# Kernel tuning notes

Hardware: AMD Instinct MI355X
Metric: run time of the kernel (lower is better)

Reference implementation:

```python
import jax, jax.numpy as jnp
import numpy as np
import math

B, S, D = 2, 2048, 1024
H, HKV, HD = 16, 4, 64
SF = 4
SD = HD // SF  # sparsity proj dim = 16
TEMP = 1.0
INIT_STD = 0.02


def rope(qk):
    # qk: [b, h, s, d]
    d = qk.shape[-1]
    theta = 1.0 / (10000.0 ** (jnp.arange(0, d, 2, dtype=jnp.float32) / d))  # [d/2]
    s = jnp.arange(qk.shape[2], dtype=jnp.float32)
    freqs = jnp.outer(s, theta)                     # [s, d/2]
    freqs = jnp.concatenate([freqs, freqs], -1)     # [s, d]
    qk1, qk2 = jnp.split(qk, 2, axis=-1)
    rot = jnp.concatenate([-qk2, qk1], -1)
    return qk * jnp.cos(freqs) + rot * jnp.sin(freqs)


def setup_inputs() -> dict:
    key = jax.random.key(0)
    ks = jax.random.split(key, 8)
    x = jax.random.normal(ks[0], (B, S, D), dtype=jnp.float32)
    Wq = jax.random.normal(ks[1], (D, D), dtype=jnp.float32) * INIT_STD
    Wk = jax.random.normal(ks[2], (HKV * HD, D), dtype=jnp.float32) * INIT_STD
    Wv = jax.random.normal(ks[3], (HKV * HD, D), dtype=jnp.float32) * INIT_STD
    Wo = jax.random.normal(ks[4], (D, D), dtype=jnp.float32) * INIT_STD
    bo = jnp.zeros((D,), dtype=jnp.float32)
    Ws = jax.random.normal(ks[5], (SD, HD), dtype=jnp.float32) * INIT_STD
    bs = jnp.zeros((SD,), dtype=jnp.float32)
    return {"x": x, "Wq": Wq, "Wk": Wk, "Wv": Wv, "Wo": Wo, "bo": bo, "Ws": Ws, "bs": bs}


def reference(x, Wq, Wk, Wv, Wo, bo, Ws, bs):
    b, s, _ = x.shape
    # projections (torch Linear: x @ W.T)
    q = (x @ Wq.T).reshape(b, s, H, HD).transpose(0, 2, 1, 3)     # [b,H,s,hd]
    k = (x @ Wk.T).reshape(b, s, HKV, HD).transpose(0, 2, 1, 3)   # [b,Hkv,s,hd]
    v = (x @ Wv.T).reshape(b, s, HKV, HD).transpose(0, 2, 1, 3)
    q = rope(q)
    k = rope(k)
    n_rep = H // HKV
    k = jnp.repeat(k, n_rep, axis=1)  # [b,H,s,hd]
    v = jnp.repeat(v, n_rep, axis=1)
    # low-rank sparsity gate
    q_sp = q @ Ws.T + bs              # [b,H,s,sd]
    k_sp = k @ Ws.T + bs
    sp_scores = jnp.einsum('bhid,bhjd->bhij', q_sp, k_sp) / math.sqrt(SD)
    gate = jax.nn.sigmoid(sp_scores / TEMP)
    attn = jnp.einsum('bhid,bhjd->bhij', q, k) / math.sqrt(HD)
    attn = attn * gate
    causal = jnp.triu(jnp.ones((s, s), dtype=bool), k=1)
    attn = jnp.where(causal, -jnp.inf, attn)
    w = jax.nn.softmax(attn, axis=-1)
    out = jnp.einsum('bhij,bhjd->bhid', w, v)               # [b,H,s,hd]
    out = out.transpose(0, 2, 1, 3).reshape(b, s, H * HD)   # [b,s,D]
    return out @ Wo.T + bo
```

## Files before the change

### kernel.cpp

```cpp
#include <hip/hip_runtime.h>
#include <math.h>

#define B_ 2
#define S_ 2048
#define D_ 1024
#define H_ 16
#define HKV_ 4
#define HD_ 64
#define SD_ 16

typedef __attribute__((ext_vector_type(8))) short bf16x8;
typedef __attribute__((ext_vector_type(4))) float f32x4;
typedef __attribute__((ext_vector_type(8))) unsigned short us8;
typedef __attribute__((ext_vector_type(4))) unsigned short us4;

__device__ __forceinline__ unsigned short f2bf(float f) {
  unsigned int u = __builtin_bit_cast(unsigned int, f);
  u += 0x7fffu + ((u >> 16) & 1u);
  return (unsigned short)(u >> 16);
}

__device__ __forceinline__ void gload16(const unsigned short* g, unsigned short* l) {
  __builtin_amdgcn_global_load_lds(
      (const __attribute__((address_space(1))) unsigned int*)g,
      (__attribute__((address_space(3))) unsigned int*)l, 16, 0, 0);
}

__global__ __launch_bounds__(256) void convert_bf16(
    const float* __restrict__ x, const float* __restrict__ wq,
    const float* __restrict__ wk, const float* __restrict__ wv,
    const float* __restrict__ wo, unsigned short* __restrict__ xb,
    unsigned short* __restrict__ wqkv, unsigned short* __restrict__ wob) {
  const int blk = blockIdx.x;
  const float* src;
  unsigned short* dst;
  int off;
  if (blk < 2048)      { src = x;  dst = xb;             off = blk * 2048; }
  else if (blk < 2560) { src = wq; dst = wqkv;           off = (blk - 2048) * 2048; }
  else if (blk < 2688) { src = wk; dst = wqkv + 1048576; off = (blk - 2560) * 2048; }
  else if (blk < 2816) { src = wv; dst = wqkv + 1310720; off = (blk - 2688) * 2048; }
  else                 { src = wo; dst = wob;            off = (blk - 2816) * 2048; }
  const int i = off + threadIdx.x * 8;
  float4 a = *(const float4*)(src + i);
  float4 b = *(const float4*)(src + i + 4);
  us8 o;
  o[0] = f2bf(a.x); o[1] = f2bf(a.y); o[2] = f2bf(a.z); o[3] = f2bf(a.w);
  o[4] = f2bf(b.x); o[5] = f2bf(b.y); o[6] = f2bf(b.z); o[7] = f2bf(b.w);
  *(us8*)(dst + i) = o;
}

__global__ __launch_bounds__(256) void gemm_bf16(
    const unsigned short* __restrict__ A, const unsigned short* __restrict__ Bm,
    const float* __restrict__ bias, float* __restrict__ C, int N) {
  __shared__ unsigned short As[128 * 64];
  __shared__ unsigned short Bs[128 * 64];
  const int tid = threadIdx.x;
  const int w = tid >> 6, lane = tid & 63;
  const int nm = lane & 15, quad = lane >> 4;
  const int m0 = blockIdx.y * 128, n0 = blockIdx.x * 128;
  const int wm = (w & 1) * 64, wn = (w >> 1) * 64;

  f32x4 acc[4][4] = {};
  int srow[4], scol[4];
#pragma unroll
  for (int it = 0; it < 4; ++it) {
    int s = it * 256 + w * 64 + lane;
    srow[it] = s >> 3;
    scol[it] = ((s & 7) ^ (srow[it] & 7)) * 8;
  }

  for (int k0 = 0; k0 < 1024; k0 += 64) {
    __syncthreads();
#pragma unroll
    for (int it = 0; it < 4; ++it)
      gload16(A + (size_t)(m0 + srow[it]) * 1024 + k0 + scol[it],
              &As[(it * 256 + w * 64) * 8]);
#pragma unroll
    for (int it = 0; it < 4; ++it)
      gload16(Bm + (size_t)(n0 + srow[it]) * 1024 + k0 + scol[it],
              &Bs[(it * 256 + w * 64) * 8]);
    __syncthreads();

#pragma unroll
    for (int ks = 0; ks < 2; ++ks) {
      bf16x8 af[4], bf[4];
      const int cq = ks * 4 + quad;
#pragma unroll
      for (int mi = 0; mi < 4; ++mi) {
        const int m = wm + mi * 16 + nm;
        af[mi] = *(const bf16x8*)&As[(m * 8 + (cq ^ (m & 7))) * 8];
      }
#pragma unroll
      for (int ni = 0; ni < 4; ++ni) {
        const int n = wn + ni * 16 + nm;
        bf[ni] = *(const bf16x8*)&Bs[(n * 8 + (cq ^ (n & 7))) * 8];
      }
#pragma unroll
      for (int mi = 0; mi < 4; ++mi)
#pragma unroll
        for (int ni = 0; ni < 4; ++ni)
          acc[mi][ni] = __builtin_amdgcn_mfma_f32_16x16x32_bf16(
              af[mi], bf[ni], acc[mi][ni], 0, 0, 0);
    }
  }

  float bv[4] = {0.f, 0.f, 0.f, 0.f};
  if (bias) {
#pragma unroll
    for (int ni = 0; ni < 4; ++ni) bv[ni] = bias[n0 + wn + ni * 16 + nm];
  }
#pragma unroll
  for (int mi = 0; mi < 4; ++mi) {
#pragma unroll
    for (int r = 0; r < 4; ++r) {
      const int row = m0 + wm + mi * 16 + quad * 4 + r;
      float* crow = C + (size_t)row * N + n0 + wn + nm;
#pragma unroll
      for (int ni = 0; ni < 4; ++ni) crow[ni * 16] = acc[mi][ni][r] + bv[ni];
    }
  }
}

__global__ __launch_bounds__(256) void rope_scatter(
    const float* __restrict__ P, const float* __restrict__ Ws,
    const float* __restrict__ bs, unsigned short* __restrict__ qh,
    unsigned short* __restrict__ kh, unsigned short* __restrict__ qsp,
    unsigned short* __restrict__ ksp) {
  __shared__ float wsl[16 * 64];
  __shared__ float bsl[16];
  __shared__ float rbuf[4][64];
  const int tid = threadIdx.x;
  const int row = blockIdx.x;
  const int b = row >> 11;
  const int s = row & 2047;
  {
    *(float4*)&wsl[tid * 4] = *(const float4*)&Ws[tid * 4];
    if (tid < 16) bsl[tid] = bs[tid];
  }
  __syncthreads();
  const int w = tid >> 6, lane = tid & 63;
  const int i = lane & 31, halfu = lane >> 5;
  const float theta = powf(10000.f, -((float)(2 * i) * (1.f / 64.f)));
  const float f = (float)s * theta;
  const float cf = cosf(f);
  const float sf = sinf(f);
  for (int slot = w; slot < 20; slot += 4) {
    float val = P[(size_t)row * 1536 + slot * 64 + lane];
    float partner = __shfl_xor(val, 32);
    float rot = halfu ? partner : -partner;
    float r = val * cf + rot * sf;
    unsigned short* dst;
    unsigned short* spdst;
    float qscale, spscale;
    if (slot < 16) {
      dst = qh + ((size_t)(b * 16 + slot) * 2048 + s) * 64;
      spdst = qsp + ((size_t)(b * 16 + slot) * 2048 + s) * 16;
      qscale = 0.125f; spscale = 0.25f;
    } else {
      int hh = slot - 16;
      dst = kh + ((size_t)(b * 4 + hh) * 2048 + s) * 64;
      spdst = ksp + ((size_t)(b * 4 + hh) * 2048 + s) * 16;
      qscale = 1.f; spscale = 1.f;
    }
    dst[lane] = f2bf(r * qscale);
    rbuf[w][lane] = r;
    int p = lane >> 4, j = lane & 15;
    float partial = 0.f;
#pragma unroll
    for (int t = 0; t < 16; ++t)
      partial += wsl[j * 64 + p * 16 + t] * rbuf[w][p * 16 + t];
    partial += __shfl_xor(partial, 16);
    partial += __shfl_xor(partial, 32);
    if (p == 0) spdst[j] = f2bf((partial + bsl[j]) * spscale);
  }
}

__global__ __launch_bounds__(256) void v_transpose(
    const float* __restrict__ proj, unsigned short* __restrict__ vt) {
  __shared__ unsigned short t_[64 * 72];
  const int bkv = blockIdx.y;
  const int s0 = blockIdx.x * 64;
  const int b = bkv >> 2, hkv = bkv & 3;
  const int tid = threadIdx.x;
  const int sl = tid >> 2;
  const int c0 = (tid & 3) * 16;
  const float* src = proj + ((size_t)b * 2048 + s0 + sl) * 1536 + 1280 + hkv * 64 + c0;
  us8 o0, o1;
#pragma unroll
  for (int t = 0; t < 8; ++t) { o0[t] = f2bf(src[t]); o1[t] = f2bf(src[8 + t]); }
  *(us8*)&t_[sl * 72 + c0] = o0;
  *(us8*)&t_[sl * 72 + c0 + 8] = o1;
  __syncthreads();
  const int d = tid >> 2;
  const int sc_ = (tid & 3) * 16;
  us8 w0, w1;
#pragma unroll
  for (int t = 0; t < 8; ++t) w0[t] = t_[(sc_ + t) * 72 + d];
#pragma unroll
  for (int t = 0; t < 8; ++t) w1[t] = t_[(sc_ + 8 + t) * 72 + d];
  unsigned short* dst = vt + (size_t)bkv * 131072 + (size_t)d * 2048 + s0 + sc_;
  *(us8*)dst = w0;
  *(us8*)(dst + 8) = w1;
}

__global__ __launch_bounds__(256) void attn_kernel(
    const unsigned short* __restrict__ qh, const unsigned short* __restrict__ kh,
    const unsigned short* __restrict__ vt, const unsigned short* __restrict__ qsp,
    const unsigned short* __restrict__ ksp, unsigned short* __restrict__ ao) {
  __shared__ unsigned short Ks[64 * 64];
  __shared__ unsigned short Vs[64 * 64];
  __shared__ unsigned short Ksp[64 * 16];
  __shared__ unsigned short Pw[4][16 * 64];

  const int tid = threadIdx.x;
  const int w = tid >> 6;
  const int lane = tid & 63;
  const int nm = lane & 15;
  const int quad = lane >> 4;
  const int bh = blockIdx.y;
  const int b = bh >> 4, h = bh & 15;
  const int hkv = h >> 2;
  const size_t kbase = (size_t)(b * 4 + hkv) * 2048 * 64;
  const size_t vbase = (size_t)(b * 4 + hkv) * 131072;
  const size_t kspb = (size_t)(b * 4 + hkv) * 2048 * 16;

  int srow_[2], scol_[2];
#pragma unroll
  for (int rd = 0; rd < 2; ++rd) {
    int Lc = rd * 256 + w * 64 + lane;
    int r = Lc >> 3;
    srow_[rd] = r;
    scol_[rd] = ((Lc & 7) ^ (r & 7)) * 8;
  }
  unsigned short* pw = &Pw[w][0];

  for (int ph = 0; ph < 2; ++ph) {
    const int qx = ph ? blockIdx.x : (31 - blockIdx.x);
    const int q0 = qx * 64;
    const int qrow0 = q0 + w * 16;

    const size_t qb = ((size_t)(b * 16 + h) * 2048 + qrow0 + nm) * 64;
    bf16x8 qa0 = *(const bf16x8*)(qh + qb + quad * 8);
    bf16x8 qa1 = *(const bf16x8*)(qh + qb + 32 + quad * 8);
    bf16x8 qspa = {0, 0, 0, 0, 0, 0, 0, 0};
    if (quad < 2)
      qspa = *(const bf16x8*)(qsp + ((size_t)(b * 16 + h) * 2048 + qrow0 + nm) * 16 + quad * 8);

    float l_r[4] = {0.f, 0.f, 0.f, 0.f};
    f32x4 O[4] = {{0.f, 0.f, 0.f, 0.f}, {0.f, 0.f, 0.f, 0.f},
                  {0.f, 0.f, 0.f, 0.f}, {0.f, 0.f, 0.f, 0.f}};

    const int ntile = qx + 1;
    for (int jt = 0; jt < ntile; ++jt) {
      const int j0 = jt * 64;
      __syncthreads();
#pragma unroll
      for (int rd = 0; rd < 2; ++rd) {
        gload16(kh + kbase + (size_t)(j0 + srow_[rd]) * 64 + scol_[rd],
                &Ks[(rd * 256 + w * 64) * 8]);
        gload16(vt + vbase + (size_t)srow_[rd] * 2048 + j0 + scol_[rd],
                &Vs[(rd * 256 + w * 64) * 8]);
      }
      if (w < 2) {
        const int Lc = w * 64 + lane;
        gload16(ksp + kspb + (size_t)(j0 + (Lc >> 1)) * 16 + (Lc & 1) * 8,
                &Ksp[w * 512]);
      }
      __syncthreads();

      const bool needmask = (j0 + 63 > qrow0);
#pragma unroll
      for (int st = 0; st < 4; ++st) {
        const int krow = st * 16 + nm;
        const int r7 = krow & 7;
        bf16x8 kb0 = *(const bf16x8*)&Ks[(krow * 8 + (quad ^ r7)) * 8];
        bf16x8 kb1 = *(const bf16x8*)&Ks[(krow * 8 + ((4 + quad) ^ r7)) * 8];
        bf16x8 gb = *(const bf16x8*)&Ksp[(krow * 2 + (quad & 1)) * 8];
        f32x4 z = {0.f, 0.f, 0.f, 0.f};
        f32x4 s = __builtin_amdgcn_mfma_f32_16x16x32_bf16(qa0, kb0, z, 0, 0, 0);
        s = __builtin_amdgcn_mfma_f32_16x16x32_bf16(qa1, kb1, s, 0, 0, 0);
        f32x4 g = __builtin_amdgcn_mfma_f32_16x16x32_bf16(qspa, gb, z, 0, 0, 0);
#pragma unroll
        for (int r = 0; r < 4; ++r) {
          float gate = 1.f / (1.f + __expf(-g[r]));
          float v = s[r] * gate;
          if (needmask) {
            const int col = j0 + st * 16 + nm;
            const int rowg = qrow0 + quad * 4 + r;
            v = (col > rowg) ? -INFINITY : v;
          }
          float p = __expf(v);
          l_r[r] += p;
          const int prow = quad * 4 + r;
          const int chunk = (st * 2 + (nm >> 3)) ^ (prow & 7);
          pw[(prow * 8 + chunk) * 8 + (nm & 7)] = f2bf(p);
        }
      }

#pragma unroll
      for (int c = 0; c < 2; ++c) {
        const int gc = c * 4 + quad;
        bf16x8 pa = *(const bf16x8*)&pw[(nm * 8 + (gc ^ (nm & 7))) * 8];
#pragma unroll
        for (int dt = 0; dt < 4; ++dt) {
          const int vrow = dt * 16 + nm;
          bf16x8 vb = *(const bf16x8*)&Vs[(vrow * 8 + (gc ^ (vrow & 7))) * 8];
          O[dt] = __builtin_amdgcn_mfma_f32_16x16x32_bf16(pa, vb, O[dt], 0, 0, 0);
        }
      }
    }

#pragma unroll
    for (int r = 0; r < 4; ++r) {
      float v = l_r[r];
      v += __shfl_xor(v, 1);
      v += __shfl_xor(v, 2);
      v += __shfl_xor(v, 4);
      v += __shfl_xor(v, 8);
      const float inv = 1.f / v;
      const int rowg = qrow0 + quad * 4 + r;
      unsigned short* orow = ao + ((size_t)b * 2048 + rowg) * 1024 + h * 64 + nm;
#pragma unroll
      for (int dt = 0; dt < 4; ++dt) orow[dt * 16] = f2bf(O[dt][r] * inv);
    }
  }
}

extern "C" void kernel_launch(void* const* d_in, const int* in_sizes, int n_in,
                              void* d_out, int out_size, void* d_ws,
                              size_t ws_size, hipStream_t stream) {
  const float* x = (const float*)d_in[0];
  const float* Wq = (const float*)d_in[1];
  const float* Wk = (const float*)d_in[2];
  const float* Wv = (const float*)d_in[3];
  const float* Wo = (const float*)d_in[4];
  const float* bo = (const float*)d_in[5];
  const float* Ws = (const float*)d_in[6];
  const float* bs = (const float*)d_in[7];
  float* out = (float*)d_out;

  char* wsb = (char*)d_ws;
  float* proj = (float*)wsb;
  unsigned short* aob = (unsigned short*)wsb;
  unsigned short* qh   = (unsigned short*)(wsb + 25165824);
  unsigned short* kh   = (unsigned short*)(wsb + 33554432);
  unsigned short* vtb  = (unsigned short*)(wsb + 35651584);
  unsigned short* qsp  = (unsigned short*)(wsb + 37748736);
  unsigned short* ksp  = (unsigned short*)(wsb + 39845888);
  unsigned short* xb   = (unsigned short*)(wsb + 40370176);
  unsigned short* wqkv = (unsigned short*)(wsb + 48758784);
  unsigned short* wob  = (unsigned short*)(wsb + 51904512);

  convert_bf16<<<dim3(3328), 256, 0, stream>>>(x, Wq, Wk, Wv, Wo, xb, wqkv, wob);
  gemm_bf16<<<dim3(12, 32), 256, 0, stream>>>(xb, wqkv, nullptr, proj, 1536);
  rope_scatter<<<dim3(4096), 256, 0, stream>>>(proj, Ws, bs, qh, kh, qsp, ksp);
  v_transpose<<<dim3(32, 8), 256, 0, stream>>>(proj, vtb);
  attn_kernel<<<dim3(16, 32), 256, 0, stream>>>(qh, kh, vtb, qsp, ksp, aob);
  gemm_bf16<<<dim3(8, 32), 256, 0, stream>>>(aob, wob, bo, out, 1024);
}
```

Baseline: 226.8 us.

## Shrink GEMM tiles, split attention into one q-tile per block, use exp2

The GEMM block tile drops from 128x128 to 64x128, with each wave now covering 64x32, which doubles the grid to fill more compute units. The attention kernel no longer has each block process two paired q-tiles in sequence; it launches one block per q-tile, interleaving small and large tiles by block index to spread the causal work. The log2(e) factor is folded into the q and sparsity-q scales so the kernel can call exp2f instead of __expf. The trade-off is less operand reuse per GEMM block and possible load imbalance between attention blocks in exchange for more parallelism.

```diff
diff --git a/kernel.cpp b/kernel.cpp
--- a/kernel.cpp
+++ b/kernel.cpp
@@ -13,6 +13,8 @@
 typedef __attribute__((ext_vector_type(4))) float f32x4;
 typedef __attribute__((ext_vector_type(8))) unsigned short us8;
 typedef __attribute__((ext_vector_type(4))) unsigned short us4;
+
+#define LOG2E 1.4426950408889634f
 
 __device__ __forceinline__ unsigned short f2bf(float f) {
   unsigned int u = __builtin_bit_cast(unsigned int, f);
@@ -52,71 +54,77 @@
 __global__ __launch_bounds__(256) void gemm_bf16(
     const unsigned short* __restrict__ A, const unsigned short* __restrict__ Bm,
     const float* __restrict__ bias, float* __restrict__ C, int N) {
-  __shared__ unsigned short As[128 * 64];
+  __shared__ unsigned short As[64 * 64];
   __shared__ unsigned short Bs[128 * 64];
   const int tid = threadIdx.x;
   const int w = tid >> 6, lane = tid & 63;
   const int nm = lane & 15, quad = lane >> 4;
-  const int m0 = blockIdx.y * 128, n0 = blockIdx.x * 128;
-  const int wm = (w & 1) * 64, wn = (w >> 1) * 64;
-
-  f32x4 acc[4][4] = {};
-  int srow[4], scol[4];
+  const int m0 = blockIdx.y * 64, n0 = blockIdx.x * 128;
+  const int wn = w * 32;
+
+  f32x4 acc[4][2] = {};
+  int arow[2], acol[2], brow[4], bcol[4];
+#pragma unroll
+  for (int it = 0; it < 2; ++it) {
+    int s = it * 256 + tid;
+    arow[it] = s >> 3;
+    acol[it] = ((s & 7) ^ (arow[it] & 7)) * 8;
+  }
 #pragma unroll
   for (int it = 0; it < 4; ++it) {
-    int s = it * 256 + w * 64 + lane;
-    srow[it] = s >> 3;
-    scol[it] = ((s & 7) ^ (srow[it] & 7)) * 8;
+    int s = it * 256 + tid;
+    brow[it] = s >> 3;
+    bcol[it] = ((s & 7) ^ (brow[it] & 7)) * 8;
   }
 
   for (int k0 = 0; k0 < 1024; k0 += 64) {
     __syncthreads();
 #pragma unroll
+    for (int it = 0; it < 2; ++it)
+      gload16(A + (size_t)(m0 + arow[it]) * 1024 + k0 + acol[it],
+              &As[(it * 256 + w * 64) * 8]);
+#pragma unroll
     for (int it = 0; it < 4; ++it)
-      gload16(A + (size_t)(m0 + srow[it]) * 1024 + k0 + scol[it],
-              &As[(it * 256 + w * 64) * 8]);
-#pragma unroll
-    for (int it = 0; it < 4; ++it)
-      gload16(Bm + (size_t)(n0 + srow[it]) * 1024 + k0 + scol[it],
+      gload16(Bm + (size_t)(n0 + brow[it]) * 1024 + k0 + bcol[it],
               &Bs[(it * 256 + w * 64) * 8]);
     __syncthreads();
 
 #pragma unroll
     for (int ks = 0; ks < 2; ++ks) {
-      bf16x8 af[4], bf[4];
       const int cq = ks * 4 + quad;
+      bf16x8 af[4], bfr[2];
 #pragma unroll
       for (int mi = 0; mi < 4; ++mi) {
-        const int m = wm + mi * 16 + nm;
+        const int m = mi * 16 + nm;
         af[mi] = *(const bf16x8*)&As[(m * 8 + (cq ^ (m & 7))) * 8];
       }
 #pragma unroll
-      for (int ni = 0; ni < 4; ++ni) {
+      for (int ni = 0; ni < 2; ++ni) {
         const int n = wn + ni * 16 + nm;
-        bf[ni] = *(const bf16x8*)&Bs[(n * 8 + (cq ^ (n & 7))) * 8];
+        bfr[ni] = *(const bf16x8*)&Bs[(n * 8 + (cq ^ (n & 7))) * 8];
       }
 #pragma unroll
       for (int mi = 0; mi < 4; ++mi)
 #pragma unroll
-        for (int ni = 0; ni < 4; ++ni)
+        for (int ni = 0; ni < 2; ++ni)
           acc[mi][ni] = __builtin_amdgcn_mfma_f32_16x16x32_bf16(
-              af[mi], bf[ni], acc[mi][ni], 0, 0, 0);
-    }
-  }
-
-  float bv[4] = {0.f, 0.f, 0.f, 0.f};
+              af[mi], bfr[ni], acc[mi][ni], 0, 0, 0);
+    }
+  }
+
+  float bv[2] = {0.f, 0.f};
   if (bias) {
 #pragma unroll
-    for (int ni = 0; ni < 4; ++ni) bv[ni] = bias[n0 + wn + ni * 16 + nm];
+    for (int ni = 0; ni < 2; ++ni) bv[ni] = bias[n0 + wn + ni * 16 + nm];
   }
 #pragma unroll
   for (int mi = 0; mi < 4; ++mi) {
 #pragma unroll
     for (int r = 0; r < 4; ++r) {
-      const int row = m0 + wm + mi * 16 + quad * 4 + r;
+      const int row = m0 + mi * 16 + quad * 4 + r;
       float* crow = C + (size_t)row * N + n0 + wn + nm;
 #pragma unroll
-      for (int ni = 0; ni < 4; ++ni) crow[ni * 16] = acc[mi][ni][r] + bv[ni];
+      for (int ni = 0; ni < 2; ++ni) crow[ni * 16] = acc[mi][ni][r] + bv[ni];
     }
   }
 }
@@ -155,7 +163,7 @@
     if (slot < 16) {
       dst = qh + ((size_t)(b * 16 + slot) * 2048 + s) * 64;
       spdst = qsp + ((size_t)(b * 16 + slot) * 2048 + s) * 16;
-      qscale = 0.125f; spscale = 0.25f;
+      qscale = 0.125f * LOG2E; spscale = 0.25f * LOG2E;
     } else {
       int hh = slot - 16;
       dst = kh + ((size_t)(b * 4 + hh) * 2048 + s) * 64;
@@ -234,95 +242,94 @@
   }
   unsigned short* pw = &Pw[w][0];
 
-  for (int ph = 0; ph < 2; ++ph) {
-    const int qx = ph ? blockIdx.x : (31 - blockIdx.x);
-    const int q0 = qx * 64;
-    const int qrow0 = q0 + w * 16;
-
-    const size_t qb = ((size_t)(b * 16 + h) * 2048 + qrow0 + nm) * 64;
-    bf16x8 qa0 = *(const bf16x8*)(qh + qb + quad * 8);
-    bf16x8 qa1 = *(const bf16x8*)(qh + qb + 32 + quad * 8);
-    bf16x8 qspa = {0, 0, 0, 0, 0, 0, 0, 0};
-    if (quad < 2)
-      qspa = *(const bf16x8*)(qsp + ((size_t)(b * 16 + h) * 2048 + qrow0 + nm) * 16 + quad * 8);
-
-    float l_r[4] = {0.f, 0.f, 0.f, 0.f};
-    f32x4 O[4] = {{0.f, 0.f, 0.f, 0.f}, {0.f, 0.f, 0.f, 0.f},
-                  {0.f, 0.f, 0.f, 0.f}, {0.f, 0.f, 0.f, 0.f}};
-
-    const int ntile = qx + 1;
-    for (int jt = 0; jt < ntile; ++jt) {
-      const int j0 = jt * 64;
-      __syncthreads();
-#pragma unroll
-      for (int rd = 0; rd < 2; ++rd) {
-        gload16(kh + kbase + (size_t)(j0 + srow_[rd]) * 64 + scol_[rd],
-                &Ks[(rd * 256 + w * 64) * 8]);
-        gload16(vt + vbase + (size_t)srow_[rd] * 2048 + j0 + scol_[rd],
-                &Vs[(rd * 256 + w * 64) * 8]);
+  const int bx = blockIdx.x;
+  const int qx = (bx & 1) ? (31 - (bx >> 1)) : (bx >> 1);
+  const int q0 = qx * 64;
+  const int qrow0 = q0 + w * 16;
+
+  const size_t qb = ((size_t)(b * 16 + h) * 2048 + qrow0 + nm) * 64;
+  bf16x8 qa0 = *(const bf16x8*)(qh + qb + quad * 8);
+  bf16x8 qa1 = *(const bf16x8*)(qh + qb + 32 + quad * 8);
+  bf16x8 qspa = {0, 0, 0, 0, 0, 0, 0, 0};
+  if (quad < 2)
+    qspa = *(const bf16x8*)(qsp + ((size_t)(b * 16 + h) * 2048 + qrow0 + nm) * 16 + quad * 8);
+
+  float l_r[4] = {0.f, 0.f, 0.f, 0.f};
+  f32x4 O[4] = {{0.f, 0.f, 0.f, 0.f}, {0.f, 0.f, 0.f, 0.f},
+                {0.f, 0.f, 0.f, 0.f}, {0.f, 0.f, 0.f, 0.f}};
+
+  const int ntile = qx + 1;
+  for (int jt = 0; jt < ntile; ++jt) {
+    const int j0 = jt * 64;
+    __syncthreads();
+#pragma unroll
+    for (int rd = 0; rd < 2; ++rd) {
+      gload16(kh + kbase + (size_t)(j0 + srow_[rd]) * 64 + scol_[rd],
+              &Ks[(rd * 256 + w * 64) * 8]);
+      gload16(vt + vbase + (size_t)srow_[rd] * 2048 + j0 + scol_[rd],
+              &Vs[(rd * 256 + w * 64) * 8]);
+    }
+    if (w < 2) {
+      const int Lc = w * 64 + lane;
+      gload16(ksp + kspb + (size_t)(j0 + (Lc >> 1)) * 16 + (Lc & 1) * 8,
+              &Ksp[w * 512]);
+    }
+    __syncthreads();
+
+    const bool needmask = (j0 + 63 > qrow0);
+#pragma unroll
+    for (int st = 0; st < 4; ++st) {
+      const int krow = st * 16 + nm;
+      const int r7 = krow & 7;
+      bf16x8 kb0 = *(const bf16x8*)&Ks[(krow * 8 + (quad ^ r7)) * 8];
+      bf16x8 kb1 = *(const bf16x8*)&Ks[(krow * 8 + ((4 + quad) ^ r7)) * 8];
+      bf16x8 gb = *(const bf16x8*)&Ksp[(krow * 2 + (quad & 1)) * 8];
+      f32x4 z = {0.f, 0.f, 0.f, 0.f};
+      f32x4 s = __builtin_amdgcn_mfma_f32_16x16x32_bf16(qa0, kb0, z, 0, 0, 0);
+      s = __builtin_amdgcn_mfma_f32_16x16x32_bf16(qa1, kb1, s, 0, 0, 0);
+      f32x4 g = __builtin_amdgcn_mfma_f32_16x16x32_bf16(qspa, gb, z, 0, 0, 0);
+#pragma unroll
+      for (int r = 0; r < 4; ++r) {
+        float gate = 1.f / (1.f + exp2f(-g[r]));
+        float v = s[r] * gate;
+        if (needmask) {
+          const int col = j0 + st * 16 + nm;
+          const int rowg = qrow0 + quad * 4 + r;
+          v = (col > rowg) ? -INFINITY : v;
+        }
+        float p = exp2f(v);
+        l_r[r] += p;
+        const int prow = quad * 4 + r;
+        const int chunk = (st * 2 + (nm >> 3)) ^ (prow & 7);
+        pw[(prow * 8 + chunk) * 8 + (nm & 7)] = f2bf(p);
       }
-      if (w < 2) {
-        const int Lc = w * 64 + lane;
-        gload16(ksp + kspb + (size_t)(j0 + (Lc >> 1)) * 16 + (Lc & 1) * 8,
-                &Ksp[w * 512]);
+    }
+
+#pragma unroll
+    for (int c = 0; c < 2; ++c) {
+      const int gc = c * 4 + quad;
+      bf16x8 pa = *(const bf16x8*)&pw[(nm * 8 + (gc ^ (nm & 7))) * 8];
+#pragma unroll
+      for (int dt = 0; dt < 4; ++dt) {
+        const int vrow = dt * 16 + nm;
+        bf16x8 vb = *(const bf16x8*)&Vs[(vrow * 8 + (gc ^ (vrow & 7))) * 8];
+        O[dt] = __builtin_amdgcn_mfma_f32_16x16x32_bf16(pa, vb, O[dt], 0, 0, 0);
       }
-      __syncthreads();
-
-      const bool needmask = (j0 + 63 > qrow0);
-#pragma unroll
-      for (int st = 0; st < 4; ++st) {
-        const int krow = st * 16 + nm;
-        const int r7 = krow & 7;
-        bf16x8 kb0 = *(const bf16x8*)&Ks[(krow * 8 + (quad ^ r7)) * 8];
-        bf16x8 kb1 = *(const bf16x8*)&Ks[(krow * 8 + ((4 + quad) ^ r7)) * 8];
-        bf16x8 gb = *(const bf16x8*)&Ksp[(krow * 2 + (quad & 1)) * 8];
-        f32x4 z = {0.f, 0.f, 0.f, 0.f};
-        f32x4 s = __builtin_amdgcn_mfma_f32_16x16x32_bf16(qa0, kb0, z, 0, 0, 0);
-        s = __builtin_amdgcn_mfma_f32_16x16x32_bf16(qa1, kb1, s, 0, 0, 0);
-        f32x4 g = __builtin_amdgcn_mfma_f32_16x16x32_bf16(qspa, gb, z, 0, 0, 0);
-#pragma unroll
-        for (int r = 0; r < 4; ++r) {
-          float gate = 1.f / (1.f + __expf(-g[r]));
-          float v = s[r] * gate;
-          if (needmask) {
-            const int col = j0 + st * 16 + nm;
-            const int rowg = qrow0 + quad * 4 + r;
-            v = (col > rowg) ? -INFINITY : v;
-          }
-          float p = __expf(v);
-          l_r[r] += p;
-          const int prow = quad * 4 + r;
-          const int chunk = (st * 2 + (nm >> 3)) ^ (prow & 7);
-          pw[(prow * 8 + chunk) * 8 + (nm & 7)] = f2bf(p);
-        }
-      }
-
-#pragma unroll
-      for (int c = 0; c < 2; ++c) {
-        const int gc = c * 4 + quad;
-        bf16x8 pa = *(const bf16x8*)&pw[(nm * 8 + (gc ^ (nm & 7))) * 8];
-#pragma unroll
-        for (int dt = 0; dt < 4; ++dt) {
-          const int vrow = dt * 16 + nm;
-          bf16x8 vb = *(const bf16x8*)&Vs[(vrow * 8 + (gc ^ (vrow & 7))) * 8];
-          O[dt] = __builtin_amdgcn_mfma_f32_16x16x32_bf16(pa, vb, O[dt], 0, 0, 0);
-        }
-      }
-    }
-
-#pragma unroll
-    for (int r = 0; r < 4; ++r) {
-      float v = l_r[r];
-      v += __shfl_xor(v, 1);
-      v += __shfl_xor(v, 2);
-      v += __shfl_xor(v, 4);
-      v += __shfl_xor(v, 8);
-      const float inv = 1.f / v;
-      const int rowg = qrow0 + quad * 4 + r;
-      unsigned short* orow = ao + ((size_t)b * 2048 + rowg) * 1024 + h * 64 + nm;
-#pragma unroll
-      for (int dt = 0; dt < 4; ++dt) orow[dt * 16] = f2bf(O[dt][r] * inv);
-    }
+    }
+  }
+
+#pragma unroll
+  for (int r = 0; r < 4; ++r) {
+    float v = l_r[r];
+    v += __shfl_xor(v, 1);
+    v += __shfl_xor(v, 2);
+    v += __shfl_xor(v, 4);
+    v += __shfl_xor(v, 8);
+    const float inv = 1.f / v;
+    const int rowg = qrow0 + quad * 4 + r;
+    unsigned short* orow = ao + ((size_t)b * 2048 + rowg) * 1024 + h * 64 + nm;
+#pragma unroll
+    for (int dt = 0; dt < 4; ++dt) orow[dt * 16] = f2bf(O[dt][r] * inv);
   }
 }
 
@@ -335,8 +342,8 @@
   const float* Wv = (const float*)d_in[3];
   const float* Wo = (const float*)d_in[4];
   const float* bo = (const float*)d_in[5];
+  const float* bs = (const float*)d_in[7];
   const float* Ws = (const float*)d_in[6];
-  const float* bs = (const float*)d_in[7];
   float* out = (float*)d_out;
 
   char* wsb = (char*)d_ws;
@@ -352,9 +359,9 @@
   unsigned short* wob  = (unsigned short*)(wsb + 51904512);
 
   convert_bf16<<<dim3(3328), 256, 0, stream>>>(x, Wq, Wk, Wv, Wo, xb, wqkv, wob);
-  gemm_bf16<<<dim3(12, 32), 256, 0, stream>>>(xb, wqkv, nullptr, proj, 1536);
+  gemm_bf16<<<dim3(12, 64), 256, 0, stream>>>(xb, wqkv, nullptr, proj, 1536);
   rope_scatter<<<dim3(4096), 256, 0, stream>>>(proj, Ws, bs, qh, kh, qsp, ksp);
   v_transpose<<<dim3(32, 8), 256, 0, stream>>>(proj, vtb);
-  attn_kernel<<<dim3(16, 32), 256, 0, stream>>>(qh, kh, vtb, qsp, ksp, aob);
-  gemm_bf16<<<dim3(8, 32), 256, 0, stream>>>(aob, wob, bo, out, 1024);
-}
+  attn_kernel<<<dim3(32, 32), 256, 0, stream>>>(qh, kh, vtb, qsp, ksp, aob);
+  gemm_bf16<<<dim3(8, 64), 256, 0, stream>>>(aob, wob, bo, out, 1024);
+}
```

After: 289.2 us. 1.28x slower.
